# Kernel tuning notes

Measured on AMD Instinct MI355X. Metric: run time of the kernel, lower is better.

The kernel has to match this reference:

```python
import jax, jax.numpy as jnp
import numpy as np

HIDDEN = 100


def gcn_conv(x, W, b, src, dst, w, n):
    # GCNConv with symmetric normalization (self-loops already appended).
    xw = x @ W                                   # [N, H]
    deg = jax.ops.segment_sum(w, dst, num_segments=n)
    dinv = jnp.where(deg > 0, jax.lax.rsqrt(deg), 0.0)
    norm = dinv[src] * w * dinv[dst]             # [E]
    agg = jax.ops.segment_sum(norm[:, None] * xw[src], dst, num_segments=n)
    return agg + b


def setup_inputs() -> dict:
    key = jax.random.key(0)
    ks = jax.random.split(key, 16)
    N, F, E, H = 100000, 128, 1600000, HIDDEN
    x = jax.random.normal(ks[0], (N, F), dtype=jnp.float32)
    edge_index = jax.random.randint(ks[1], (2, E), 0, N, dtype=jnp.int64)
    edge_weight = jax.random.uniform(ks[2], (E,), dtype=jnp.float32)
    sF = 1.0 / np.sqrt(F)
    sH2 = 1.0 / np.sqrt(2 * H)
    sH = 1.0 / np.sqrt(H)
    inp = {
        "x": x, "edge_index": edge_index, "edge_weight": edge_weight,
        "Wcz": jax.random.normal(ks[3], (F, H), jnp.float32) * sF,
        "bcz": jnp.zeros((H,), jnp.float32),
        "Wcr": jax.random.normal(ks[4], (F, H), jnp.float32) * sF,
        "bcr": jnp.zeros((H,), jnp.float32),
        "Wch": jax.random.normal(ks[5], (F, H), jnp.float32) * sF,
        "bch": jnp.zeros((H,), jnp.float32),
        "Wlz": jax.random.normal(ks[6], (2 * H, H), jnp.float32) * sH2,
        "blz": jnp.zeros((H,), jnp.float32),
        "Wlr": jax.random.normal(ks[7], (2 * H, H), jnp.float32) * sH2,
        "blr": jnp.zeros((H,), jnp.float32),
        "Wlh": jax.random.normal(ks[8], (2 * H, H), jnp.float32) * sH2,
        "blh": jnp.zeros((H,), jnp.float32),
        "Wout": jax.random.normal(ks[9], (H, 1), jnp.float32) * sH,
        "bout": jnp.zeros((1,), jnp.float32),
    }
    return inp


def reference(x, edge_index, edge_weight,
              Wcz, bcz, Wcr, bcr, Wch, bch,
              Wlz, blz, Wlr, blr, Wlh, blh,
              Wout, bout):
    N = x.shape[0]
    # add self-loops with weight 1 (GCNConv default)
    loop = jnp.arange(N, dtype=edge_index.dtype)
    src = jnp.concatenate([edge_index[0], loop])
    dst = jnp.concatenate([edge_index[1], loop])
    w = jnp.concatenate([edge_weight, jnp.ones((N,), edge_weight.dtype)])

    H0 = jnp.zeros((N, HIDDEN), x.dtype)  # TGCN initial hidden state

    cz = gcn_conv(x, Wcz, bcz, src, dst, w, N)
    Z = jax.nn.sigmoid(jnp.concatenate([cz, H0], axis=1) @ Wlz + blz)

    cr = gcn_conv(x, Wcr, bcr, src, dst, w, N)
    R = jax.nn.sigmoid(jnp.concatenate([cr, H0], axis=1) @ Wlr + blr)

    ch = gcn_conv(x, Wch, bch, src, dst, w, N)
    Ht = jnp.tanh(jnp.concatenate([ch, H0 * R], axis=1) @ Wlh + blh)

    Hn = Z * H0 + (1.0 - Z) * Ht
    h = jax.nn.relu(Hn)
    return h @ Wout + bout
```

## Files before the change

kernel.cpp:

```cpp
#include <hip/hip_runtime.h>

#define FEAT 128
#define HID  100

typedef __attribute__((ext_vector_type(8))) short short8;
typedef __attribute__((ext_vector_type(4))) float f32x4;

__device__ __forceinline__ unsigned short f2bf(float f) {
    union { float f; unsigned int u; } v; v.f = f;
    unsigned int r = v.u + 0x7fffu + ((v.u >> 16) & 1u);
    return (unsigned short)(r >> 16);
}

__device__ __forceinline__ int get_edge(const void* ei, int f64, long long pos) {
    return f64 ? (int)((const long long*)ei)[pos] : ((const int*)ei)[pos];
}

__global__ void k_detect(const void* ei, int* flag) {
    int t = threadIdx.x;
    const int* p = (const int*)ei;
    unsigned long long b = __ballot(p[2 * t + 1] == 0);
    if (t == 0) *flag = (b == ~0ull) ? 1 : 0;
}

__global__ __launch_bounds__(256)
void k_cvt(const float* __restrict__ x, uint4* __restrict__ xb, int n8) {
    int stride = gridDim.x * blockDim.x;
    for (int i = blockIdx.x * blockDim.x + threadIdx.x; i < n8; i += stride) {
        float4 a = *(const float4*)(x + (size_t)i * 8);
        float4 b = *(const float4*)(x + (size_t)i * 8 + 4);
        uint4 o;
        o.x = f2bf(a.x) | ((unsigned)f2bf(a.y) << 16);
        o.y = f2bf(a.z) | ((unsigned)f2bf(a.w) << 16);
        o.z = f2bf(b.x) | ((unsigned)f2bf(b.y) << 16);
        o.w = f2bf(b.z) | ((unsigned)f2bf(b.w) << 16);
        xb[i] = o;
    }
}

__global__ void k_deg2(const void* ei, const int* flag, int* counts, int* rank, int E) {
    int e = blockIdx.x * blockDim.x + threadIdx.x;
    if (e >= E) return;
    int f64 = *flag;
    int d = get_edge(ei, f64, (long long)E + e);
    rank[e] = atomicAdd(&counts[d], 1);
}

__global__ void k_scan1(const int* counts, int* offs, int* partials, int N) {
    __shared__ int lds[1024];
    int t = threadIdx.x;
    int idx = blockIdx.x * 1024 + t;
    int v = (idx < N) ? counts[idx] : 0;
    lds[t] = v;
    __syncthreads();
    for (int off = 1; off < 1024; off <<= 1) {
        int tv = (t >= off) ? lds[t - off] : 0;
        __syncthreads();
        lds[t] += tv;
        __syncthreads();
    }
    if (idx < N) offs[idx] = lds[t] - v;
    if (t == 1023) partials[blockIdx.x] = lds[1023];
}

__global__ void k_scan2(int* partials, int nb) {
    __shared__ int lds[128];
    int t = threadIdx.x;
    int v = (t < nb) ? partials[t] : 0;
    lds[t] = v;
    __syncthreads();
    for (int off = 1; off < 128; off <<= 1) {
        int tv = (t >= off) ? lds[t - off] : 0;
        __syncthreads();
        lds[t] += tv;
        __syncthreads();
    }
    if (t < nb) partials[t] = lds[t] - v;
}

__global__ void k_scan3(int* offs, const int* partials, int N) {
    int idx = blockIdx.x * 1024 + threadIdx.x;
    if (idx < N) offs[idx] += partials[blockIdx.x];
}

__global__ void k_fill2(const void* ei, const float* w, const int* flag,
                        const int* offs, const int* rank, int2* csr, int E) {
    int e = blockIdx.x * blockDim.x + threadIdx.x;
    if (e >= E) return;
    int f64 = *flag;
    int s = get_edge(ei, f64, e);
    int d = get_edge(ei, f64, (long long)E + e);
    int pos = offs[d] + rank[e];
    csr[pos] = make_int2(s, __float_as_int(w[e]));
}

__global__ __launch_bounds__(256)
void k_degsum(const int2* __restrict__ csr, const int* __restrict__ offs,
              const int* __restrict__ counts, float* __restrict__ dinv, int N) {
    int t = threadIdx.x;
    int sub = t & 15;
    long long node = (long long)blockIdx.x * 16 + (t >> 4);
    if (node >= N) return;
    int rs = offs[node], cnt = counts[node];
    float s = 0.f;
    for (int i = sub; i < cnt; i += 16) s += __int_as_float(csr[rs + i].y);
    s += __shfl_xor(s, 1);
    s += __shfl_xor(s, 2);
    s += __shfl_xor(s, 4);
    s += __shfl_xor(s, 8);
    if (sub == 0) dinv[node] = rsqrtf(1.f + s);
}

__global__ __launch_bounds__(256)
void k_agg4(const unsigned short* __restrict__ xb, const float* __restrict__ dinv,
            const int* __restrict__ offs, const int* __restrict__ counts,
            const int2* __restrict__ csr, unsigned short* __restrict__ aggx, int N) {
    int wid  = __builtin_amdgcn_readfirstlane(threadIdx.x >> 6);
    int lane = threadIdx.x & 63;
    long long node = (long long)blockIdx.x * 4 + wid;
    if (node >= N) return;
    int q  = lane >> 3;
    int fl = lane & 7;
    float acc[16];
#pragma unroll
    for (int j = 0; j < 16; j++) acc[j] = 0.f;
    int rs  = offs[node];
    int cnt = counts[node];
    for (int i = q; i < cnt; i += 8) {
        int2 e = csr[rs + i];
        float nr = __int_as_float(e.y) * dinv[e.x];
        const uint4* xp = (const uint4*)(xb + (size_t)e.x * FEAT + fl * 16);
        uint4 v0 = xp[0];
        uint4 v1 = xp[1];
        const unsigned* u0 = &v0.x;
        const unsigned* u1 = &v1.x;
#pragma unroll
        for (int j = 0; j < 4; j++) {
            acc[2*j]     += nr * __uint_as_float(u0[j] << 16);
            acc[2*j + 1] += nr * __uint_as_float(u0[j] & 0xffff0000u);
            acc[8 + 2*j]     += nr * __uint_as_float(u1[j] << 16);
            acc[8 + 2*j + 1] += nr * __uint_as_float(u1[j] & 0xffff0000u);
        }
    }
#pragma unroll
    for (int j = 0; j < 16; j++) {
        acc[j] += __shfl_xor(acc[j], 8);
        acc[j] += __shfl_xor(acc[j], 16);
        acc[j] += __shfl_xor(acc[j], 32);
    }
    if (q == 0) {
        float dn = dinv[node];
        const uint4* xs = (const uint4*)(xb + (size_t)node * FEAT + fl * 16);
        uint4 s0 = xs[0];
        uint4 s1 = xs[1];
        const unsigned* u0 = &s0.x;
        const unsigned* u1 = &s1.x;
#pragma unroll
        for (int j = 0; j < 4; j++) {
            acc[2*j]     += dn * __uint_as_float(u0[j] << 16);
            acc[2*j + 1] += dn * __uint_as_float(u0[j] & 0xffff0000u);
            acc[8 + 2*j]     += dn * __uint_as_float(u1[j] << 16);
            acc[8 + 2*j + 1] += dn * __uint_as_float(u1[j] & 0xffff0000u);
        }
        uint4 o0, o1;
        unsigned* p0 = &o0.x;
        unsigned* p1 = &o1.x;
#pragma unroll
        for (int j = 0; j < 4; j++) {
            p0[j] = f2bf(acc[2*j] * dn)     | ((unsigned)f2bf(acc[2*j+1] * dn) << 16);
            p1[j] = f2bf(acc[8+2*j] * dn)   | ((unsigned)f2bf(acc[8+2*j+1] * dn) << 16);
        }
        uint4* op = (uint4*)(aggx + (size_t)node * FEAT + fl * 16);
        op[0] = o0;
        op[1] = o1;
    }
}

__global__ __launch_bounds__(256)
void k_fold2(const float* __restrict__ Wcz, const float* __restrict__ bcz,
             const float* __restrict__ Wch, const float* __restrict__ bch,
             const float* __restrict__ Wlz, const float* __restrict__ blz,
             const float* __restrict__ Wlh, const float* __restrict__ blh,
             const float* __restrict__ Wout,
             unsigned short* __restrict__ WB, float* __restrict__ bfold_ext,
             float* __restrict__ WoutZ) {
    int idx = blockIdx.x * 256 + threadIdx.x;
    if (idx < FEAT * 256) {
        int k = idx >> 8, n = idx & 255;
        float val = 0.f;
        if (n < HID) {
            for (int m = 0; m < HID; m++) val += Wcz[k * HID + m] * Wlz[m * HID + n];
        } else if (n >= 128 && n < 128 + HID) {
            int c = n - 128;
            for (int m = 0; m < HID; m++) val += Wch[k * HID + m] * Wlh[m * HID + c];
        }
        int ni = n >> 4, lc = n & 15, ks = k >> 5, hi = (k >> 3) & 3, j = k & 7;
        WB[(((ni * 4 + ks) * 64 + hi * 16 + lc) << 3) + j] = f2bf(val);
    } else if (idx < FEAT * 256 + 256) {
        int c = idx - FEAT * 256;
        float v = 0.f;
        if (c < HID) {
            v = blz[c];
            for (int j = 0; j < HID; j++) v += bcz[j] * Wlz[j * HID + c];
        } else if (c >= 128 && c < 128 + HID) {
            int cc = c - 128;
            v = blh[cc];
            for (int j = 0; j < HID; j++) v += bch[j] * Wlh[j * HID + cc];
        }
        bfold_ext[c] = v;
    } else if (idx < FEAT * 256 + 256 + 128) {
        int c = idx - FEAT * 256 - 256;
        WoutZ[c] = (c < HID) ? Wout[c] : 0.f;
    }
}

__global__ __launch_bounds__(256)
void k_post3(const unsigned short* __restrict__ aggx, const unsigned short* __restrict__ WB,
             const float* __restrict__ bfold_ext, const float* __restrict__ WoutZ,
             const float* __restrict__ bout, float* __restrict__ out, int N) {
    __shared__ unsigned short At[64 * 136];
    __shared__ float red[64 * 4];
    int t = threadIdx.x;
    int lane = t & 63;
    int w = __builtin_amdgcn_readfirstlane(t >> 6);
    long long base = (long long)blockIdx.x * 64;

    for (int it = 0; it < 4; it++) {
        int idx = it * 256 + t;
        int row = idx >> 4, c16 = idx & 15;
        long long grow = base + row;
        uint4 v = make_uint4(0u, 0u, 0u, 0u);
        if (grow < N) v = *(const uint4*)(aggx + grow * FEAT + c16 * 8);
        *(uint4*)(At + row * 136 + c16 * 8) = v;
    }
    __syncthreads();

    int l15 = lane & 15, lhi = lane >> 4;
    int tadd = 2 * w;
    f32x4 acc[4][4];
#pragma unroll
    for (int ti = 0; ti < 4; ti++)
#pragma unroll
        for (int mi = 0; mi < 4; mi++) acc[ti][mi] = (f32x4)0.f;

    const int tiles[4] = {tadd, tadd + 1, tadd + 8, tadd + 9};
#pragma unroll
    for (int ks = 0; ks < 4; ks++) {
        short8 a[4];
#pragma unroll
        for (int mi = 0; mi < 4; mi++)
            a[mi] = *(const short8*)(At + (mi * 16 + l15) * 136 + ks * 32 + lhi * 8);
        short8 b[4];
#pragma unroll
        for (int ti = 0; ti < 4; ti++)
            b[ti] = *(const short8*)(WB + (((tiles[ti] * 4 + ks) * 64 + lane) << 3));
#pragma unroll
        for (int ti = 0; ti < 4; ti++)
#pragma unroll
            for (int mi = 0; mi < 4; mi++)
                acc[ti][mi] = __builtin_amdgcn_mfma_f32_16x16x32_bf16(
                    a[mi], b[ti], acc[ti][mi], 0, 0, 0);
    }

    float partial[4][4];
#pragma unroll
    for (int mi = 0; mi < 4; mi++)
#pragma unroll
        for (int r = 0; r < 4; r++) partial[mi][r] = 0.f;
#pragma unroll
    for (int d = 0; d < 2; d++) {
        int zcol = (tadd + d) * 16 + l15;
        float bz = bfold_ext[zcol];
        float bh = bfold_ext[zcol + 128];
        float wo = WoutZ[zcol];
#pragma unroll
        for (int mi = 0; mi < 4; mi++)
#pragma unroll
            for (int r = 0; r < 4; r++) {
                float az = acc[d][mi][r] + bz;
                float ah = acc[d + 2][mi][r] + bh;
                float z  = 1.f / (1.f + expf(-az));
                float ht = tanhf(ah);
                float h  = (1.f - z) * ht;
                h = h > 0.f ? h : 0.f;
                partial[mi][r] += h * wo;
            }
    }
#pragma unroll
    for (int mi = 0; mi < 4; mi++)
#pragma unroll
        for (int r = 0; r < 4; r++) {
            float p = partial[mi][r];
            p += __shfl_xor(p, 1);
            p += __shfl_xor(p, 2);
            p += __shfl_xor(p, 4);
            p += __shfl_xor(p, 8);
            partial[mi][r] = p;
        }
    if (l15 == 0) {
#pragma unroll
        for (int mi = 0; mi < 4; mi++)
#pragma unroll
            for (int r = 0; r < 4; r++)
                red[(mi * 16 + lhi * 4 + r) * 4 + w] = partial[mi][r];
    }
    __syncthreads();
    if (t < 64) {
        long long node = base + t;
        if (node < N)
            out[node] = red[t * 4] + red[t * 4 + 1] + red[t * 4 + 2] + red[t * 4 + 3]
                      + bout[0];
    }
}

extern "C" void kernel_launch(void* const* d_in, const int* in_sizes, int n_in,
                              void* d_out, int out_size, void* d_ws, size_t ws_size,
                              hipStream_t stream) {
    const float* x    = (const float*)d_in[0];
    const void*  ei   = d_in[1];
    const float* ew   = (const float*)d_in[2];
    const float* Wcz  = (const float*)d_in[3];
    const float* bcz  = (const float*)d_in[4];
    const float* Wch  = (const float*)d_in[7];
    const float* bch  = (const float*)d_in[8];
    const float* Wlz  = (const float*)d_in[9];
    const float* blz  = (const float*)d_in[10];
    const float* Wlh  = (const float*)d_in[13];
    const float* blh  = (const float*)d_in[14];
    const float* Wout = (const float*)d_in[15];
    const float* bout = (const float*)d_in[16];
    float* out = (float*)d_out;

    int N = in_sizes[0] / FEAT;
    int E = in_sizes[2];

    char* p = (char*)d_ws;
    auto alloc = [&](size_t bytes) -> char* {
        char* r = p;
        p += (bytes + 255) & ~(size_t)255;
        return r;
    };
    int*            flag      = (int*)  alloc(256);
    float*          dinv      = (float*)alloc((size_t)N * 4);
    int*            counts    = (int*)  alloc((size_t)N * 4);
    int*            offs      = (int*)  alloc((size_t)N * 4);
    int*            partials  = (int*)  alloc(512);
    int2*           csr       = (int2*) alloc((size_t)E * 8);
    unsigned short* xb        = (unsigned short*)alloc((size_t)N * FEAT * 2);
    unsigned short* aggx      = (unsigned short*)alloc((size_t)N * FEAT * 2);
    unsigned short* WB        = (unsigned short*)alloc((size_t)FEAT * 256 * 2);
    float*          bfold_ext = (float*)alloc(256 * 4);
    float*          WoutZ     = (float*)alloc(128 * 4);
    int*            rank      = (int*)aggx;

    int nb = (N + 1023) / 1024;

    k_detect<<<1, 64, 0, stream>>>(ei, flag);
    hipMemsetAsync(counts, 0, (size_t)N * 4, stream);
    k_cvt<<<1024, 256, 0, stream>>>(x, (uint4*)xb, N * FEAT / 8);
    k_deg2<<<(E + 255) / 256, 256, 0, stream>>>(ei, flag, counts, rank, E);
    k_scan1<<<nb, 1024, 0, stream>>>(counts, offs, partials, N);
    k_scan2<<<1, 128, 0, stream>>>(partials, nb);
    k_scan3<<<nb, 1024, 0, stream>>>(offs, partials, N);
    k_fill2<<<(E + 255) / 256, 256, 0, stream>>>(ei, ew, flag, offs, rank, csr, E);
    k_degsum<<<(N + 15) / 16, 256, 0, stream>>>(csr, offs, counts, dinv, N);
    k_agg4<<<(N + 3) / 4, 256, 0, stream>>>(xb, dinv, offs, counts, csr, aggx, N);
    k_fold2<<<(FEAT * 256 + 256 + 128 + 255) / 256, 256, 0, stream>>>(
        Wcz, bcz, Wch, bch, Wlz, blz, Wlh, blh, Wout, WB, bfold_ext, WoutZ);
    k_post3<<<(N + 63) / 64, 256, 0, stream>>>(aggx, WB, bfold_ext, WoutZ, bout, out, N);
}
```

Measured before the change: 352.6 us.

## Fuse cvt with weight folding, inline dtype detect, pad atomic counters, self-loop in CSR

Merges the bf16 conversion and weight-folding kernels into one launch and drops the separate dtype-detect kernel by having each edge kernel ballot-detect int64 indices itself. Per-node degree counters are padded to one cache line each to cut atomic contention, with the padded buffer aliased into the CSR storage. The self-loop is written as an extra CSR entry so aggregation handles it in the main loop. Rank and CSR writes use nontemporal stores. This saves launches and atomic contention at the cost of a larger memset (N*128 bytes) and an extra per-node CSR slot.

```diff
diff --git a/kernel.cpp b/kernel.cpp
--- a/kernel.cpp
+++ b/kernel.cpp
@@ -2,6 +2,7 @@
 
 #define FEAT 128
 #define HID  100
+#define CPAD 32
 
 typedef __attribute__((ext_vector_type(8))) short short8;
 typedef __attribute__((ext_vector_type(4))) float f32x4;
@@ -16,175 +17,37 @@
     return f64 ? (int)((const long long*)ei)[pos] : ((const int*)ei)[pos];
 }
 
-__global__ void k_detect(const void* ei, int* flag) {
-    int t = threadIdx.x;
+__device__ __forceinline__ int detect_f64(const void* ei) {
     const int* p = (const int*)ei;
-    unsigned long long b = __ballot(p[2 * t + 1] == 0);
-    if (t == 0) *flag = (b == ~0ull) ? 1 : 0;
+    unsigned long long b = __ballot(p[2 * (threadIdx.x & 63) + 1] == 0);
+    return b == ~0ull;
 }
 
 __global__ __launch_bounds__(256)
-void k_cvt(const float* __restrict__ x, uint4* __restrict__ xb, int n8) {
-    int stride = gridDim.x * blockDim.x;
-    for (int i = blockIdx.x * blockDim.x + threadIdx.x; i < n8; i += stride) {
-        float4 a = *(const float4*)(x + (size_t)i * 8);
-        float4 b = *(const float4*)(x + (size_t)i * 8 + 4);
-        uint4 o;
-        o.x = f2bf(a.x) | ((unsigned)f2bf(a.y) << 16);
-        o.y = f2bf(a.z) | ((unsigned)f2bf(a.w) << 16);
-        o.z = f2bf(b.x) | ((unsigned)f2bf(b.y) << 16);
-        o.w = f2bf(b.z) | ((unsigned)f2bf(b.w) << 16);
-        xb[i] = o;
-    }
-}
-
-__global__ void k_deg2(const void* ei, const int* flag, int* counts, int* rank, int E) {
-    int e = blockIdx.x * blockDim.x + threadIdx.x;
-    if (e >= E) return;
-    int f64 = *flag;
-    int d = get_edge(ei, f64, (long long)E + e);
-    rank[e] = atomicAdd(&counts[d], 1);
-}
-
-__global__ void k_scan1(const int* counts, int* offs, int* partials, int N) {
-    __shared__ int lds[1024];
-    int t = threadIdx.x;
-    int idx = blockIdx.x * 1024 + t;
-    int v = (idx < N) ? counts[idx] : 0;
-    lds[t] = v;
-    __syncthreads();
-    for (int off = 1; off < 1024; off <<= 1) {
-        int tv = (t >= off) ? lds[t - off] : 0;
-        __syncthreads();
-        lds[t] += tv;
-        __syncthreads();
-    }
-    if (idx < N) offs[idx] = lds[t] - v;
-    if (t == 1023) partials[blockIdx.x] = lds[1023];
-}
-
-__global__ void k_scan2(int* partials, int nb) {
-    __shared__ int lds[128];
-    int t = threadIdx.x;
-    int v = (t < nb) ? partials[t] : 0;
-    lds[t] = v;
-    __syncthreads();
-    for (int off = 1; off < 128; off <<= 1) {
-        int tv = (t >= off) ? lds[t - off] : 0;
-        __syncthreads();
-        lds[t] += tv;
-        __syncthreads();
-    }
-    if (t < nb) partials[t] = lds[t] - v;
-}
-
-__global__ void k_scan3(int* offs, const int* partials, int N) {
-    int idx = blockIdx.x * 1024 + threadIdx.x;
-    if (idx < N) offs[idx] += partials[blockIdx.x];
-}
-
-__global__ void k_fill2(const void* ei, const float* w, const int* flag,
-                        const int* offs, const int* rank, int2* csr, int E) {
-    int e = blockIdx.x * blockDim.x + threadIdx.x;
-    if (e >= E) return;
-    int f64 = *flag;
-    int s = get_edge(ei, f64, e);
-    int d = get_edge(ei, f64, (long long)E + e);
-    int pos = offs[d] + rank[e];
-    csr[pos] = make_int2(s, __float_as_int(w[e]));
-}
-
-__global__ __launch_bounds__(256)
-void k_degsum(const int2* __restrict__ csr, const int* __restrict__ offs,
-              const int* __restrict__ counts, float* __restrict__ dinv, int N) {
-    int t = threadIdx.x;
-    int sub = t & 15;
-    long long node = (long long)blockIdx.x * 16 + (t >> 4);
-    if (node >= N) return;
-    int rs = offs[node], cnt = counts[node];
-    float s = 0.f;
-    for (int i = sub; i < cnt; i += 16) s += __int_as_float(csr[rs + i].y);
-    s += __shfl_xor(s, 1);
-    s += __shfl_xor(s, 2);
-    s += __shfl_xor(s, 4);
-    s += __shfl_xor(s, 8);
-    if (sub == 0) dinv[node] = rsqrtf(1.f + s);
-}
-
-__global__ __launch_bounds__(256)
-void k_agg4(const unsigned short* __restrict__ xb, const float* __restrict__ dinv,
-            const int* __restrict__ offs, const int* __restrict__ counts,
-            const int2* __restrict__ csr, unsigned short* __restrict__ aggx, int N) {
-    int wid  = __builtin_amdgcn_readfirstlane(threadIdx.x >> 6);
-    int lane = threadIdx.x & 63;
-    long long node = (long long)blockIdx.x * 4 + wid;
-    if (node >= N) return;
-    int q  = lane >> 3;
-    int fl = lane & 7;
-    float acc[16];
-#pragma unroll
-    for (int j = 0; j < 16; j++) acc[j] = 0.f;
-    int rs  = offs[node];
-    int cnt = counts[node];
-    for (int i = q; i < cnt; i += 8) {
-        int2 e = csr[rs + i];
-        float nr = __int_as_float(e.y) * dinv[e.x];
-        const uint4* xp = (const uint4*)(xb + (size_t)e.x * FEAT + fl * 16);
-        uint4 v0 = xp[0];
-        uint4 v1 = xp[1];
-        const unsigned* u0 = &v0.x;
-        const unsigned* u1 = &v1.x;
-#pragma unroll
-        for (int j = 0; j < 4; j++) {
-            acc[2*j]     += nr * __uint_as_float(u0[j] << 16);
-            acc[2*j + 1] += nr * __uint_as_float(u0[j] & 0xffff0000u);
-            acc[8 + 2*j]     += nr * __uint_as_float(u1[j] << 16);
-            acc[8 + 2*j + 1] += nr * __uint_as_float(u1[j] & 0xffff0000u);
-        }
-    }
-#pragma unroll
-    for (int j = 0; j < 16; j++) {
-        acc[j] += __shfl_xor(acc[j], 8);
-        acc[j] += __shfl_xor(acc[j], 16);
-        acc[j] += __shfl_xor(acc[j], 32);
-    }
-    if (q == 0) {
-        float dn = dinv[node];
-        const uint4* xs = (const uint4*)(xb + (size_t)node * FEAT + fl * 16);
-        uint4 s0 = xs[0];
-        uint4 s1 = xs[1];
-        const unsigned* u0 = &s0.x;
-        const unsigned* u1 = &s1.x;
-#pragma unroll
-        for (int j = 0; j < 4; j++) {
-            acc[2*j]     += dn * __uint_as_float(u0[j] << 16);
-            acc[2*j + 1] += dn * __uint_as_float(u0[j] & 0xffff0000u);
-            acc[8 + 2*j]     += dn * __uint_as_float(u1[j] << 16);
-            acc[8 + 2*j + 1] += dn * __uint_as_float(u1[j] & 0xffff0000u);
-        }
-        uint4 o0, o1;
-        unsigned* p0 = &o0.x;
-        unsigned* p1 = &o1.x;
-#pragma unroll
-        for (int j = 0; j < 4; j++) {
-            p0[j] = f2bf(acc[2*j] * dn)     | ((unsigned)f2bf(acc[2*j+1] * dn) << 16);
-            p1[j] = f2bf(acc[8+2*j] * dn)   | ((unsigned)f2bf(acc[8+2*j+1] * dn) << 16);
-        }
-        uint4* op = (uint4*)(aggx + (size_t)node * FEAT + fl * 16);
-        op[0] = o0;
-        op[1] = o1;
-    }
-}
-
-__global__ __launch_bounds__(256)
-void k_fold2(const float* __restrict__ Wcz, const float* __restrict__ bcz,
-             const float* __restrict__ Wch, const float* __restrict__ bch,
-             const float* __restrict__ Wlz, const float* __restrict__ blz,
-             const float* __restrict__ Wlh, const float* __restrict__ blh,
-             const float* __restrict__ Wout,
-             unsigned short* __restrict__ WB, float* __restrict__ bfold_ext,
-             float* __restrict__ WoutZ) {
-    int idx = blockIdx.x * 256 + threadIdx.x;
+void k_cvtfold(const float* __restrict__ x, uint4* __restrict__ xb, int n8,
+               const float* __restrict__ Wcz, const float* __restrict__ bcz,
+               const float* __restrict__ Wch, const float* __restrict__ bch,
+               const float* __restrict__ Wlz, const float* __restrict__ blz,
+               const float* __restrict__ Wlh, const float* __restrict__ blh,
+               const float* __restrict__ Wout,
+               unsigned short* __restrict__ WB, float* __restrict__ bfold_ext,
+               float* __restrict__ WoutZ) {
+    const int CVTB = 1024;
+    if (blockIdx.x < CVTB) {
+        int stride = CVTB * 256;
+        for (int i = blockIdx.x * 256 + threadIdx.x; i < n8; i += stride) {
+            float4 a = *(const float4*)(x + (size_t)i * 8);
+            float4 b = *(const float4*)(x + (size_t)i * 8 + 4);
+            uint4 o;
+            o.x = f2bf(a.x) | ((unsigned)f2bf(a.y) << 16);
+            o.y = f2bf(a.z) | ((unsigned)f2bf(a.w) << 16);
+            o.z = f2bf(b.x) | ((unsigned)f2bf(b.y) << 16);
+            o.w = f2bf(b.z) | ((unsigned)f2bf(b.w) << 16);
+            xb[i] = o;
+        }
+        return;
+    }
+    int idx = (blockIdx.x - CVTB) * 256 + threadIdx.x;
     if (idx < FEAT * 256) {
         int k = idx >> 8, n = idx & 255;
         float val = 0.f;
@@ -211,6 +74,139 @@
     } else if (idx < FEAT * 256 + 256 + 128) {
         int c = idx - FEAT * 256 - 256;
         WoutZ[c] = (c < HID) ? Wout[c] : 0.f;
+    }
+}
+
+__global__ void k_deg2p(const void* ei, int* countsPad, int* rank, int E) {
+    int f64 = detect_f64(ei);
+    int e = blockIdx.x * blockDim.x + threadIdx.x;
+    if (e >= E) return;
+    int d = get_edge(ei, f64, (long long)E + e);
+    int r = atomicAdd(&countsPad[d * CPAD], 1);
+    __builtin_nontemporal_store(r, &rank[e]);
+}
+
+__global__ void k_scan1c(const int* countsPad, int* offs, int* partials,
+                         int* cnt, int N) {
+    __shared__ int lds[1024];
+    int t = threadIdx.x;
+    int idx = blockIdx.x * 1024 + t;
+    int v = (idx < N) ? countsPad[idx * CPAD] + 1 : 0;
+    if (idx < N) cnt[idx] = v;
+    lds[t] = v;
+    __syncthreads();
+    for (int off = 1; off < 1024; off <<= 1) {
+        int tv = (t >= off) ? lds[t - off] : 0;
+        __syncthreads();
+        lds[t] += tv;
+        __syncthreads();
+    }
+    if (idx < N) offs[idx] = lds[t] - v;
+    if (t == 1023) partials[blockIdx.x] = lds[1023];
+}
+
+__global__ void k_scan2(int* partials, int nb) {
+    __shared__ int lds[128];
+    int t = threadIdx.x;
+    int v = (t < nb) ? partials[t] : 0;
+    lds[t] = v;
+    __syncthreads();
+    for (int off = 1; off < 128; off <<= 1) {
+        int tv = (t >= off) ? lds[t - off] : 0;
+        __syncthreads();
+        lds[t] += tv;
+        __syncthreads();
+    }
+    if (t < nb) partials[t] = lds[t] - v;
+}
+
+__global__ void k_scan3(int* offs, const int* partials, int N) {
+    int idx = blockIdx.x * 1024 + threadIdx.x;
+    if (idx < N) offs[idx] += partials[blockIdx.x];
+}
+
+__global__ void k_fill2(const void* ei, const float* w,
+                        const int* offs, const int* rank, int2* csr, int E) {
+    int f64 = detect_f64(ei);
+    int e = blockIdx.x * blockDim.x + threadIdx.x;
+    if (e >= E) return;
+    int s = get_edge(ei, f64, e);
+    int d = get_edge(ei, f64, (long long)E + e);
+    int pos = offs[d] + rank[e];
+    long long val = ((long long)__float_as_int(w[e]) << 32) | (unsigned)s;
+    __builtin_nontemporal_store(val, (long long*)&csr[pos]);
+}
+
+__global__ __launch_bounds__(256)
+void k_degsum(int2* __restrict__ csr, const int* __restrict__ offs,
+              const int* __restrict__ cnt, float* __restrict__ dinv, int N) {
+    int t = threadIdx.x;
+    int sub = t & 15;
+    long long node = (long long)blockIdx.x * 16 + (t >> 4);
+    if (node >= N) return;
+    int rs = offs[node], c = cnt[node];
+    float s = 0.f;
+    for (int i = sub; i < c - 1; i += 16) s += __int_as_float(csr[rs + i].y);
+    s += __shfl_xor(s, 1);
+    s += __shfl_xor(s, 2);
+    s += __shfl_xor(s, 4);
+    s += __shfl_xor(s, 8);
+    if (sub == 0) {
+        dinv[node] = rsqrtf(1.f + s);
+        csr[rs + c - 1] = make_int2((int)node, __float_as_int(1.0f));
+    }
+}
+
+__global__ __launch_bounds__(256)
+void k_agg4(const unsigned short* __restrict__ xb, const float* __restrict__ dinv,
+            const int* __restrict__ offs, const int* __restrict__ cnt,
+            const int2* __restrict__ csr, unsigned short* __restrict__ aggx, int N) {
+    int wid  = __builtin_amdgcn_readfirstlane(threadIdx.x >> 6);
+    int lane = threadIdx.x & 63;
+    long long node = (long long)blockIdx.x * 4 + wid;
+    if (node >= N) return;
+    int q  = lane >> 3;
+    int fl = lane & 7;
+    float acc[16];
+#pragma unroll
+    for (int j = 0; j < 16; j++) acc[j] = 0.f;
+    int rs = offs[node];
+    int c  = cnt[node];
+    for (int i = q; i < c; i += 8) {
+        int2 e = csr[rs + i];
+        float nr = __int_as_float(e.y) * dinv[e.x];
+        const uint4* xp = (const uint4*)(xb + (size_t)e.x * FEAT + fl * 16);
+        uint4 v0 = xp[0];
+        uint4 v1 = xp[1];
+        const unsigned* u0 = &v0.x;
+        const unsigned* u1 = &v1.x;
+#pragma unroll
+        for (int j = 0; j < 4; j++) {
+            acc[2*j]         += nr * __uint_as_float(u0[j] << 16);
+            acc[2*j + 1]     += nr * __uint_as_float(u0[j] & 0xffff0000u);
+            acc[8 + 2*j]     += nr * __uint_as_float(u1[j] << 16);
+            acc[8 + 2*j + 1] += nr * __uint_as_float(u1[j] & 0xffff0000u);
+        }
+    }
+#pragma unroll
+    for (int j = 0; j < 16; j++) {
+        acc[j] += __shfl_xor(acc[j], 8);
+        acc[j] += __shfl_xor(acc[j], 16);
+        acc[j] += __shfl_xor(acc[j], 32);
+    }
+    if (q == 0) {
+        float dn = dinv[node];
+        uint4 o0, o1;
+        unsigned* p0 = &o0.x;
+        unsigned* p1 = &o1.x;
+#pragma unroll
+        for (int j = 0; j < 4; j++) {
+            p0[j] = f2bf(acc[2*j] * dn)   | ((unsigned)f2bf(acc[2*j+1] * dn) << 16);
+            p1[j] = f2bf(acc[8+2*j] * dn) | ((unsigned)f2bf(acc[8+2*j+1] * dn) << 16);
+        }
+        uint4* op = (uint4*)(aggx + (size_t)node * FEAT + fl * 16);
+        op[0] = o0;
+        op[1] = o1;
     }
 }
 
@@ -340,32 +336,34 @@
         p += (bytes + 255) & ~(size_t)255;
         return r;
     };
-    int*            flag      = (int*)  alloc(256);
     float*          dinv      = (float*)alloc((size_t)N * 4);
-    int*            counts    = (int*)  alloc((size_t)N * 4);
+    int*            cnt       = (int*)  alloc((size_t)N * 4);
     int*            offs      = (int*)  alloc((size_t)N * 4);
     int*            partials  = (int*)  alloc(512);
-    int2*           csr       = (int2*) alloc((size_t)E * 8);
+    size_t          csr_bytes = (size_t)(E + N) * 8;
+    size_t          cpad_bytes= (size_t)N * CPAD * 4;
+    int2*           csr       = (int2*) alloc(csr_bytes > cpad_bytes ? csr_bytes
+                                                                     : cpad_bytes);
     unsigned short* xb        = (unsigned short*)alloc((size_t)N * FEAT * 2);
     unsigned short* aggx      = (unsigned short*)alloc((size_t)N * FEAT * 2);
     unsigned short* WB        = (unsigned short*)alloc((size_t)FEAT * 256 * 2);
     float*          bfold_ext = (float*)alloc(256 * 4);
     float*          WoutZ     = (float*)alloc(128 * 4);
-    int*            rank      = (int*)aggx;
+    int* countsPad = (int*)csr;
+    int* rank      = (int*)aggx;
 
     int nb = (N + 1023) / 1024;
 
-    k_detect<<<1, 64, 0, stream>>>(ei, flag);
-    hipMemsetAsync(counts, 0, (size_t)N * 4, stream);
-    k_cvt<<<1024, 256, 0, stream>>>(x, (uint4*)xb, N * FEAT / 8);
-    k_deg2<<<(E + 255) / 256, 256, 0, stream>>>(ei, flag, counts, rank, E);
-    k_scan1<<<nb, 1024, 0, stream>>>(counts, offs, partials, N);
+    hipMemsetAsync(countsPad, 0, cpad_bytes, stream);
+    k_cvtfold<<<1024 + (FEAT * 256 + 256 + 128 + 255) / 256, 256, 0, stream>>>(
+        x, (uint4*)xb, N * FEAT / 8,
+        Wcz, bcz, Wch, bch, Wlz, blz, Wlh, blh, Wout, WB, bfold_ext, WoutZ);
+    k_deg2p<<<(E + 255) / 256, 256, 0, stream>>>(ei, countsPad, rank, E);
+    k_scan1c<<<nb, 1024, 0, stream>>>(countsPad, offs, partials, cnt, N);
     k_scan2<<<1, 128, 0, stream>>>(partials, nb);
     k_scan3<<<nb, 1024, 0, stream>>>(offs, partials, N);
-    k_fill2<<<(E + 255) / 256, 256, 0, stream>>>(ei, ew, flag, offs, rank, csr, E);
-    k_degsum<<<(N + 15) / 16, 256, 0, stream>>>(csr, offs, counts, dinv, N);
-    k_agg4<<<(N + 3) / 4, 256, 0, stream>>>(xb, dinv, offs, counts, csr, aggx, N);
-    k_fold2<<<(FEAT * 256 + 256 + 128 + 255) / 256, 256, 0, stream>>>(
-        Wcz, bcz, Wch, bch, Wlz, blz, Wlh, blh, Wout, WB, bfold_ext, WoutZ);
+    k_fill2<<<(E + 255) / 256, 256, 0, stream>>>(ei, ew, offs, rank, csr, E);
+    k_degsum<<<(N + 15) / 16, 256, 0, stream>>>(csr, offs, cnt, dinv, N);
+    k_agg4<<<(N + 3) / 4, 256, 0, stream>>>(xb, dinv, offs, cnt, csr, aggx, N);
     k_post3<<<(N + 63) / 64, 256, 0, stream>>>(aggx, WB, bfold_ext, WoutZ, bout, out, N);
 }
```

Result: no change. 358.2 us (+1.6%).
